# Optimization experiments

Hardware: AMD Instinct MI355X
Metric: run time of the kernel (lower is better)

Reference implementation:

```python
import jax, jax.numpy as jnp
import numpy as np

B, S = 32, 128
NUM_Q, NUM_C = 10000, 256
DIM_K, DIM_E, DIM_CORRECT = 128, 128, 50


def setup_inputs() -> dict:
    key = jax.random.key(0)
    ks = jax.random.split(key, 16)
    w = lambda k, shape: jax.random.normal(k, shape, dtype=jnp.float32) * 0.05
    z = lambda n: jnp.zeros((n,), jnp.float32)
    # q_matrix: sparse binary concept-question map with small smoothing (typical LPKT gamma)
    q_matrix = (jax.random.uniform(ks[4], (NUM_Q + 10, NUM_C)) < 0.03).astype(jnp.float32) + 0.03
    return {
        'e_data': jax.random.randint(ks[0], (B, S), 0, NUM_Q),
        'at_data': jax.random.randint(ks[1], (B, S), 0, 3600),
        'it_data': jax.random.randint(ks[2], (B, S), 0, 43200),
        'a_data': jax.random.uniform(ks[3], (B, S), dtype=jnp.float32),
        'q_matrix': q_matrix,
        'e_E': w(ks[5], (NUM_Q + 10, DIM_K)),
        'at_E': w(ks[6], (3610, DIM_K)),
        'it_E': w(ks[7], (43210, DIM_K)),
        'W1': w(ks[8], (DIM_E + DIM_K + DIM_CORRECT, DIM_K)), 'b1': z(DIM_K),
        'W2': w(ks[9], (4 * DIM_K, DIM_K)), 'b2': z(DIM_K),
        'W3': w(ks[10], (4 * DIM_K, DIM_K)), 'b3': z(DIM_K),
        'W4': w(ks[11], (3 * DIM_K, DIM_K)), 'b4': z(DIM_K),
        'W5': w(ks[12], (DIM_E + DIM_K, DIM_K)), 'b5': z(DIM_K),
        'h0': w(ks[13], (NUM_C, DIM_K)),
    }


def reference(e_data, at_data, it_data, a_data, q_matrix, e_E, at_E, it_E,
              W1, b1, W2, b2, W3, b3, W4, b4, W5, b5, h0):
    Bn, Sn = e_data.shape
    K = W1.shape[1]
    e_emb = e_E[e_data]          # [B,S,K]
    at_emb = at_E[at_data]       # [B,S,K]
    it_emb = it_E[it_data]       # [B,S,K]
    a_rep = jnp.broadcast_to(a_data[:, :, None], (Bn, Sn, DIM_CORRECT))
    all_learning = jnp.concatenate([e_emb, at_emb, a_rep], -1) @ W1 + b1  # [B,S,K]
    q_all = q_matrix[e_data]     # [B,S,C]

    h_init = jnp.broadcast_to(h0, (Bn,) + h0.shape)              # [B,C,K]
    h_tilde_init = jnp.einsum('bc,bck->bk', q_all[:, 0], h_init)  # [B,K]
    learning_init = jnp.zeros((Bn, K), all_learning.dtype)

    xs = jax.tree.map(lambda x: jnp.swapaxes(x, 0, 1),
                      (q_all[:, :-1], q_all[:, 1:], all_learning[:, :-1],
                       it_emb[:, :-1], e_emb[:, 1:]))

    def step(carry, x):
        h, h_tilde, learning_pre = carry
        q_e, q_next, learning, it, e_next = x
        zcat = jnp.concatenate([learning_pre, it, learning, h_tilde], -1)  # [B,4K]
        lg = jnp.tanh(zcat @ W2 + b2)
        gamma_l = jax.nn.sigmoid(zcat @ W3 + b3)
        LG = gamma_l * (lg + 1.0) * 0.5                                    # [B,K]
        LG_tilde = q_e[:, :, None] * LG[:, None, :]                        # [B,C,K] (dropout=eval identity)
        gf_in = jnp.concatenate([h,
                                 jnp.broadcast_to(LG[:, None, :], h.shape),
                                 jnp.broadcast_to(it[:, None, :], h.shape)], -1)
        gamma_f = jax.nn.sigmoid(gf_in @ W4 + b4)                          # [B,C,K]
        h_new = LG_tilde + gamma_f * h
        h_tilde_new = jnp.einsum('bc,bck->bk', q_next, h_new)             # [B,K]
        y = jax.nn.sigmoid(jnp.concatenate([e_next, h_tilde_new], -1) @ W5 + b5).sum(-1) / K
        return (h_new, h_tilde_new, learning), y

    _, ys = jax.lax.scan(step, (h_init, h_tilde_init, learning_init), xs)  # ys: [S-1,B]
    pred = jnp.concatenate([jnp.zeros((Bn, 1), ys.dtype), ys.T], axis=1)    # [B,S]
    return pred
```

## Files before the change

kernel.cpp:

```cpp
#include <hip/hip_runtime.h>
#include <stdint.h>

#define S   128
#define NB  32
#define NC  256
#define DK  128
#define NSL 4
#define HROW 264

typedef __bf16 bf16x8 __attribute__((ext_vector_type(8)));
typedef float  f32x16 __attribute__((ext_vector_type(16)));
typedef unsigned int u32x4 __attribute__((ext_vector_type(4)));
typedef unsigned int u32x2 __attribute__((ext_vector_type(2)));
typedef _Float16 f16x2 __attribute__((ext_vector_type(2)));
static_assert(sizeof(bf16x8) == 16, "bf16x8 size");
static_assert(sizeof(f16x2) == 4, "f16x2 size");

#define OFF_AL   0
#define OFF_HT   OFF_AL
#define OFF_P2   524288
#define OFF_P3   1044480
#define OFF_PS   1564672
#define OFF_PY   2084864
#define OFF_WT5  2654208
#define OFF_CM   2670592

__device__ __forceinline__ float v_exp2(float x){ float r; asm("v_exp_f32 %0, %1" : "=v"(r) : "v"(x)); return r; }
__device__ __forceinline__ float v_rcp (float x){ float r; asm("v_rcp_f32 %0, %1" : "=v"(r) : "v"(x)); return r; }
__device__ __forceinline__ float sigm(float x){ return v_rcp(1.0f + v_exp2(x * -1.4426950408889634f)); }
__device__ __forceinline__ uint32_t pkbf(float lo, float hi){
  uint32_t r; asm("v_cvt_pk_bf16_f32 %0, %1, %2" : "=v"(r) : "v"(lo), "v"(hi)); return r;
}
__device__ __forceinline__ float bfhi(uint32_t w){ return __builtin_bit_cast(float, w & 0xffff0000u); }
__device__ __forceinline__ uint32_t pkh(float a, float b){
  return __builtin_bit_cast(uint32_t, __builtin_amdgcn_cvt_pkrtz(a, b));
}
__device__ __forceinline__ float fdot2u(uint32_t a, uint32_t b, float c){
  return __builtin_amdgcn_fdot2(__builtin_bit_cast(f16x2, a), __builtin_bit_cast(f16x2, b), c, false);
}
__device__ __forceinline__ void barrier_lgkm(){
  asm volatile("s_waitcnt lgkmcnt(0)" ::: "memory");
  __builtin_amdgcn_s_barrier();
}
#define NLOG2E (-1.4426950408889634f)

__global__ __launch_bounds__(512) void k0_al(
    const int* __restrict__ e_data, const int* __restrict__ at_data,
    const float* __restrict__ a_data, const float* __restrict__ e_E,
    const float* __restrict__ at_E, const float* __restrict__ W1,
    const float* __restrict__ b1, float* __restrict__ ws)
{
  __shared__ float ein[32][128];
  __shared__ float atin[32][128];
  int b = blockIdx.x >> 2, q4 = blockIdx.x & 3, t0 = q4 * 32;
  for (int idx = threadIdx.x; idx < 32 * 128; idx += 512) {
    int r = idx >> 7, j = idx & 127;
    int ev  = e_data [b * S + t0 + r];
    int atv = at_data[b * S + t0 + r];
    ein [r][j] = e_E [ev  * DK + j];
    atin[r][j] = at_E[atv * DK + j];
  }
  __syncthreads();
  int j = threadIdx.x & 127, tq = threadIdx.x >> 7;
  float w1s = 0.f;
  for (int d = 0; d < 50; ++d) w1s += W1[(256 + d) * DK + j];
  float acc[8];
#pragma unroll
  for (int u = 0; u < 8; ++u) {
    int t = t0 + tq * 8 + u;
    acc[u] = b1[j] + a_data[b * S + t] * w1s;
  }
  for (int k = 0; k < 128; ++k) {
    float w = W1[k * DK + j];
#pragma unroll
    for (int u = 0; u < 8; ++u) acc[u] += ein[tq * 8 + u][k] * w;
  }
  for (int k = 0; k < 128; ++k) {
    float w = W1[(128 + k) * DK + j];
#pragma unroll
    for (int u = 0; u < 8; ++u) acc[u] += atin[tq * 8 + u][k] * w;
  }
#pragma unroll
  for (int u = 0; u < 8; ++u)
    ws[OFF_AL + (b * S + t0 + tq * 8 + u) * DK + j] = acc[u];
}

__global__ __launch_bounds__(256) void kT_tr(const float* __restrict__ W5, float* __restrict__ ws)
{
  int idx = blockIdx.x * 256 + threadIdx.x;
  int j = idx >> 7, k = idx & 127;
  ws[OFF_WT5 + j * DK + k] = W5[(128 + k) * DK + j];
}

__global__ __launch_bounds__(512) void k1_pre(
    const int* __restrict__ e_data, const int* __restrict__ it_data,
    const float* __restrict__ it_E, const float* __restrict__ e_E,
    const float* __restrict__ W2, const float* __restrict__ b2,
    const float* __restrict__ W3, const float* __restrict__ b3,
    const float* __restrict__ W4, const float* __restrict__ b4,
    const float* __restrict__ W5, const float* __restrict__ b5,
    float* __restrict__ ws)
{
  __shared__ float als[33][128];
  __shared__ float its[32][128];
  __shared__ float ens[32][128];
  int b = blockIdx.x >> 2, sh = blockIdx.x & 3, s0 = sh * 32;
  for (int idx = threadIdx.x; idx < 33 * 128; idx += 512) {
    int r = idx >> 7, j = idx & 127;
    int srow = s0 - 1 + r;
    als[r][j] = (srow >= 0) ? ws[OFF_AL + (b * S + srow) * DK + j] : 0.f;
  }
  for (int idx = threadIdx.x; idx < 32 * 128; idx += 512) {
    int r = idx >> 7, j = idx & 127;
    int itv = it_data[b * S + s0 + r];
    its[r][j] = it_E[itv * DK + j];
    int sg = s0 + r + 1; if (sg > 127) sg = 127;
    int ev = e_data[b * S + sg];
    ens[r][j] = e_E[ev * DK + j];
  }
  __syncthreads();
  int j = threadIdx.x & 127, sq = threadIdx.x >> 7;
  float p2[8], p3[8], pS[8], pY[8];
#pragma unroll
  for (int u = 0; u < 8; ++u) { p2[u] = b2[j]; p3[u] = b3[j]; pS[u] = b4[j]; pY[u] = b5[j]; }
  for (int k = 0; k < 128; ++k) {
    float w2 = W2[k * DK + j], w3 = W3[k * DK + j];
#pragma unroll
    for (int u = 0; u < 8; ++u) { float v = als[sq * 8 + u][k]; p2[u] += v * w2; p3[u] += v * w3; }
  }
  for (int k = 0; k < 128; ++k) {
    float w2 = W2[(128 + k) * DK + j], w3 = W3[(128 + k) * DK + j], w4 = W4[(256 + k) * DK + j];
#pragma unroll
    for (int u = 0; u < 8; ++u) { float v = its[sq * 8 + u][k]; p2[u] += v * w2; p3[u] += v * w3; pS[u] += v * w4; }
  }
  for (int k = 0; k < 128; ++k) {
    float w2 = W2[(256 + k) * DK + j], w3 = W3[(256 + k) * DK + j];
#pragma unroll
    for (int u = 0; u < 8; ++u) { float v = als[sq * 8 + u + 1][k]; p2[u] += v * w2; p3[u] += v * w3; }
  }
  for (int k = 0; k < 128; ++k) {
    float w5 = W5[k * DK + j];
#pragma unroll
    for (int u = 0; u < 8; ++u) pY[u] += ens[sq * 8 + u][k] * w5;
  }
#pragma unroll
  for (int u = 0; u < 8; ++u) {
    int s = s0 + sq * 8 + u;
    if (s < 127) {
      int o = (b * 127 + s) * DK + j;
      ws[OFF_P2 + o] = p2[u]; ws[OFF_P3 + o] = p3[u];
      ws[OFF_PS + o] = pS[u]; ws[OFF_PY + o] = pY[u];
    }
  }
}

__global__ __launch_bounds__(512, 2) void kmain(
    const int* __restrict__ e_data, const float* __restrict__ qmat,
    const float* __restrict__ W2, const float* __restrict__ W3,
    const float* __restrict__ W4, const float* __restrict__ h0,
    float* ws)
{
  __shared__ char     hsb[64 * HROW];
  __shared__ u32x4    W4B[4][8][64];
  __shared__ uint32_t W4Lh[64][128];
  __shared__ float    qbuf[3][64];
  __shared__ float    PST[2][3][128];
  __shared__ uint32_t htldp[64];
  __shared__ uint32_t LGp[64];

  const int bx = blockIdx.x;
  const int b = bx & 31, slice = bx >> 5;
  const int tid = threadIdx.x;
  const int lane = tid & 63, wv = tid >> 6;
  const int ct = wv >> 2, jt = wv & 3;
  const int lo = lane & 31, hi = lane >> 5;
  const int jA = tid >> 2, am = (tid >> 1) & 1, akh = tid & 1;
  const int jloc = jt * 32 + lo;

  uint32_t* cm32 = (uint32_t*)(ws + OFF_CM) + (size_t)b * 2048;

  uint32_t Awh[32];
  {
    const float* Wm = am ? W3 : W2;
#pragma unroll
    for (int i = 0; i < 32; ++i) {
      float w0 = Wm[(384 + akh * 64 + 2 * i) * DK + jA];
      float w1 = Wm[(384 + akh * 64 + 2 * i + 1) * DK + jA];
      Awh[i] = pkh(w0, w1);
    }
  }
  float hm[16];
#pragma unroll
  for (int r = 0; r < 16; ++r) {
    int cl = ct * 32 + (r & 3) + 8 * (r >> 2) + 4 * hi;
    hm[r] = h0[(slice * 64 + cl) * DK + jloc];
  }

  {
    uint32_t* w4b = (uint32_t*)&W4B[0][0][0];
#pragma unroll
    for (int it = 0; it < 16; ++it) {
      int idx = tid + it * 512;
      int w = idx & 3, l = (idx >> 2) & 63, kk = (idx >> 8) & 7, jb = idx >> 11;
      int llo = l & 31, lhi = l >> 5;
      int row = kk * 16 + lhi * 8 + 2 * w, col = jb * 32 + llo;
      w4b[idx] = pkbf(W4[row * DK + col], W4[(row + 1) * DK + col]);
    }
  }
#pragma unroll
  for (int it = 0; it < 16; ++it) {
    int idx = tid + it * 512, kp = idx >> 7, jj = idx & 127;
    W4Lh[kp][jj] = pkh(W4[(128 + 2 * kp) * DK + jj], W4[(128 + 2 * kp + 1) * DK + jj]);
  }
  if (tid < 64) {
    qbuf[0][tid] = qmat[e_data[b * S + 0] * NC + slice * 64 + tid];
    qbuf[1][tid] = qmat[e_data[b * S + 1] * NC + slice * 64 + tid];
  }
  if (tid < 384) {
    int mm = tid >> 7, jj = tid & 127;
    int off = (mm == 0) ? OFF_P2 : (mm == 1) ? OFF_P3 : OFF_PS;
    PST[0][mm][jj] = ws[off + (b * 127 + 0) * DK + jj];
  }
#pragma unroll
  for (int r = 0; r < 16; ++r) {
    int cl = ct * 32 + (r & 3) + 8 * (r >> 2) + 4 * hi;
    *(uint16_t*)(hsb + cl * HROW + jloc * 2) = (uint16_t)pkbf(hm[r], 0.f);
  }
  __syncthreads();

  {
    float ht = 0.f;
#pragma unroll
    for (int r = 0; r < 16; ++r) {
      int cl = ct * 32 + (r & 3) + 8 * (r >> 2) + 4 * hi;
      ht += qbuf[0][cl] * hm[r];
    }
    ht += __shfl_xor(ht, 32);
    if (hi == 0)
      __hip_atomic_store(&cm32[1 * 1024 + (slice * 2 + ct) * 128 + jloc],
                         pkbf(0.f, ht) | 1u, __ATOMIC_RELAXED, __HIP_MEMORY_SCOPE_AGENT);
  }

  float vreg = 0.f;

#pragma unroll 1
  for (int s = 0; s < S - 1; ++s) {
    const int par = s & 1;

    float qld = 0.f, pld = 0.f;
    if (tid >= 448)
      qld = qmat[e_data[b * S + min(s + 2, S - 1)] * NC + slice * 64 + (tid - 448)];
    if (tid >= 128) {
      int mm = (tid - 128) >> 7, jj = tid & 127;
      int off = (mm == 0) ? OFF_P2 : (mm == 1) ? OFF_P3 : OFF_PS;
      pld = ws[off + (b * 127 + min(s + 1, 126)) * DK + jj];
    }

    f32x16 acc;
#pragma unroll
    for (int r = 0; r < 16; ++r) acc[r] = 0.f;
    {
      const char* base = hsb + (ct * 32 + lo) * HROW;
#pragma unroll
      for (int kk = 0; kk < 8; ++kk) {
        u32x2 a0 = *(const u32x2*)(base + kk * 32 + hi * 16);
        u32x2 a1 = *(const u32x2*)(base + kk * 32 + hi * 16 + 8);
        u32x4 af4; af4[0] = a0[0]; af4[1] = a0[1]; af4[2] = a1[0]; af4[3] = a1[1];
        u32x4 bfr = W4B[jt][kk][lane];
        acc = __builtin_amdgcn_mfma_f32_32x32x16_bf16(
            __builtin_bit_cast(bf16x8, af4), __builtin_bit_cast(bf16x8, bfr), acc, 0, 0, 0);
      }
    }

    if (wv < 2) {
      const uint32_t tgt = (uint32_t)(s + 1);
      const uint32_t* src = cm32 + ((s + 1) & 1) * 1024;
      uint32_t g[8];
      for (;;) {
        uint32_t tsum = 0;
#pragma unroll
        for (int p = 0; p < 8; ++p) {
          g[p] = __hip_atomic_load(&src[p * 128 + wv * 64 + lane],
                                   __ATOMIC_RELAXED, __HIP_MEMORY_SCOPE_AGENT);
          tsum += g[p] & 0xffffu;
        }
        if (__all(tsum == 8u * tgt)) break;
        __builtin_amdgcn_s_sleep(1);
      }
      float v = 0.f;
#pragma unroll
      for (int p = 0; p < 8; ++p) v += bfhi(g[p]);
      vreg = v;
      float vn = __shfl_xor(v, 1);
      if (!(lane & 1)) htldp[wv * 32 + (lane >> 1)] = pkh(v, vn);
    }
    barrier_lgkm();

    if (slice == 0 && s > 0 && wv < 2)
      ws[OFF_HT + (b * 127 + (s - 1)) * DK + wv * 64 + lane] = vreg;
    {
      float p0 = 0.f, p1 = 0.f, p2a = 0.f, p3a = 0.f;
#pragma unroll
      for (int t = 0; t < 8; ++t) {
        p0  = fdot2u(htldp[akh * 32 + 4 * t + 0], Awh[4 * t + 0], p0);
        p1  = fdot2u(htldp[akh * 32 + 4 * t + 1], Awh[4 * t + 1], p1);
        p2a = fdot2u(htldp[akh * 32 + 4 * t + 2], Awh[4 * t + 2], p2a);
        p3a = fdot2u(htldp[akh * 32 + 4 * t + 3], Awh[4 * t + 3], p3a);
      }
      float p = (p0 + p1) + (p2a + p3a);
      p += __shfl_xor(p, 1);
      float po = __shfl_xor(p, 2);
      float v2 = am ? po : p;
      float v3 = am ? p : po;
      v2 += PST[par][0][jA];
      v3 += PST[par][1][jA];
      float lg = sigm(v3) * sigm(2.f * v2);
      float lgn = __shfl_xor(lg, 4);
      if ((tid & 7) == 0) LGp[tid >> 3] = pkh(lg, lgn);
    }
    barrier_lgkm();

    if (tid >= 448) qbuf[(s + 2) % 3][tid - 448] = qld;
    if (tid >= 128) {
      int mm = (tid - 128) >> 7, jj = tid & 127;
      PST[(s + 1) & 1][mm][jj] = pld;
    }
    {
      float q0 = 0.f, q1 = 0.f, q2 = 0.f, q3 = 0.f;
#pragma unroll
      for (int t = 0; t < 8; ++t) {
        q0 = fdot2u(LGp[hi * 32 + 4 * t + 0], W4Lh[hi * 32 + 4 * t + 0][jloc], q0);
        q1 = fdot2u(LGp[hi * 32 + 4 * t + 1], W4Lh[hi * 32 + 4 * t + 1][jloc], q1);
        q2 = fdot2u(LGp[hi * 32 + 4 * t + 2], W4Lh[hi * 32 + 4 * t + 2][jloc], q2);
        q3 = fdot2u(LGp[hi * 32 + 4 * t + 3], W4Lh[hi * 32 + 4 * t + 3][jloc], q3);
      }
      float pB = (q0 + q1) + (q2 + q3);
      pB += __shfl_xor(pB, 32);
      float sb = PST[par][2][jloc] + pB;
      float sn = sb * NLOG2E;
      f16x2 l2 = __builtin_bit_cast(f16x2, LGp[jloc >> 1]);
      float lgj = (float)l2[jloc & 1];
      const float* qc = &qbuf[s % 3][0];
      const float* qn = &qbuf[(s + 1) % 3][0];
      float ht = 0.f;
#pragma unroll
      for (int q4 = 0; q4 < 4; ++q4) {
        int cbase = ct * 32 + 8 * q4 + 4 * hi;
        float4 qe4 = *(const float4*)&qc[cbase];
        float4 qn4 = *(const float4*)&qn[cbase];
#pragma unroll
        for (int rr = 0; rr < 4; ++rr) {
          int r = 4 * q4 + rr;
          float qe = (rr == 0) ? qe4.x : (rr == 1) ? qe4.y : (rr == 2) ? qe4.z : qe4.w;
          float qq = (rr == 0) ? qn4.x : (rr == 1) ? qn4.y : (rr == 2) ? qn4.z : qn4.w;
          int cl = cbase + rr;
          float g = v_rcp(1.0f + v_exp2(fmaf(acc[r], NLOG2E, sn)));
          float hn = fmaf(g, hm[r], qe * lgj);
          hm[r] = hn; ht = fmaf(qq, hn, ht);
          *(uint16_t*)(hsb + cl * HROW + jloc * 2) = (uint16_t)pkbf(hn, 0.f);
        }
      }
      ht += __shfl_xor(ht, 32);
      if (hi == 0)
        __hip_atomic_store(&cm32[(s & 1) * 1024 + (slice * 2 + ct) * 128 + jloc],
                           pkbf(0.f, ht) | (uint32_t)(s + 2),
                           __ATOMIC_RELAXED, __HIP_MEMORY_SCOPE_AGENT);
    }
    barrier_lgkm();
  }

  if (slice == 0 && wv < 2) {
    const uint32_t* src = cm32 + 0 * 1024;
    uint32_t g[8];
    for (;;) {
      uint32_t tsum = 0;
#pragma unroll
      for (int p = 0; p < 8; ++p) {
        g[p] = __hip_atomic_load(&src[p * 128 + wv * 64 + lane],
                                 __ATOMIC_RELAXED, __HIP_MEMORY_SCOPE_AGENT);
        tsum += g[p] & 0xffffu;
      }
      if (__all(tsum == 8u * 128u)) break;
      __builtin_amdgcn_s_sleep(1);
    }
    float v = 0.f;
#pragma unroll
    for (int p = 0; p < 8; ++p) v += bfhi(g[p]);
    ws[OFF_HT + (b * 127 + 126) * DK + wv * 64 + lane] = v;
  }
}

__global__ __launch_bounds__(128) void k2_y(const float* __restrict__ ws, float* __restrict__ out)
{
  __shared__ float hts[8][128];
  __shared__ float part[2][8];
  int b = blockIdx.x >> 4, ch = blockIdx.x & 15, s0 = ch * 8;
  int j = threadIdx.x;
#pragma unroll
  for (int u = 0; u < 8; ++u) {
    int s = s0 + u;
    hts[u][j] = (s < 127) ? ws[OFF_HT + (b * 127 + s) * DK + j] : 0.f;
  }
  __syncthreads();
  float acc[8];
#pragma unroll
  for (int u = 0; u < 8; ++u) {
    int s = s0 + u;
    acc[u] = (s < 127) ? ws[OFF_PY + (b * 127 + s) * DK + j] : 0.f;
  }
  const float4* w5 = (const float4*)(ws + OFF_WT5 + j * DK);
#pragma unroll 8
  for (int i = 0; i < 32; ++i) {
    float4 w = w5[i];
#pragma unroll
    for (int u = 0; u < 8; ++u) {
      float4 h4 = *(const float4*)&hts[u][4 * i];
      acc[u] += w.x * h4.x + w.y * h4.y + w.z * h4.z + w.w * h4.w;
    }
  }
#pragma unroll
  for (int u = 0; u < 8; ++u) {
    float v = sigm(acc[u]);
#pragma unroll
    for (int off = 32; off >= 1; off >>= 1) v += __shfl_xor(v, off);
    if ((j & 63) == 0) part[j >> 6][u] = v;
  }
  __syncthreads();
  if (j < 8) {
    int s = s0 + j;
    if (s < 127) out[b * S + s + 1] = (part[0][j] + part[1][j]) * (1.0f / 128.0f);
  }
  if (j == 0 && ch == 0) out[b * S] = 0.f;
}

extern "C" void kernel_launch(void* const* d_in, const int* in_sizes, int n_in,
                              void* d_out, int out_size, void* d_ws, size_t ws_size,
                              hipStream_t stream)
{
  (void)in_sizes; (void)n_in; (void)out_size; (void)ws_size;
  const int*   e_data  = (const int*)  d_in[0];
  const int*   at_data = (const int*)  d_in[1];
  const int*   it_data = (const int*)  d_in[2];
  const float* a_data  = (const float*)d_in[3];
  const float* qmat    = (const float*)d_in[4];
  const float* e_E     = (const float*)d_in[5];
  const float* at_E    = (const float*)d_in[6];
  const float* it_E    = (const float*)d_in[7];
  const float* W1 = (const float*)d_in[8];  const float* b1 = (const float*)d_in[9];
  const float* W2 = (const float*)d_in[10]; const float* b2 = (const float*)d_in[11];
  const float* W3 = (const float*)d_in[12]; const float* b3 = (const float*)d_in[13];
  const float* W4 = (const float*)d_in[14]; const float* b4 = (const float*)d_in[15];
  const float* W5 = (const float*)d_in[16]; const float* b5 = (const float*)d_in[17];
  const float* h0 = (const float*)d_in[18];
  float* ws  = (float*)d_ws;
  float* out = (float*)d_out;

  hipMemsetAsync((char*)d_ws + (size_t)OFF_CM * 4, 0, (size_t)NB * 2 * 8 * 128 * 4, stream);

  k0_al <<<128, 512, 0, stream>>>(e_data, at_data, a_data, e_E, at_E, W1, b1, ws);
  kT_tr <<<64, 256, 0, stream>>>(W5, ws);
  k1_pre<<<128, 512, 0, stream>>>(e_data, it_data, it_E, e_E, W2, b2, W3, b3, W4, b4, W5, b5, ws);
  kmain <<<128, 512, 0, stream>>>(e_data, qmat, W2, W3, W4, h0, ws);
  k2_y  <<<512, 128, 0, stream>>>(ws, out);
}
```

Measured before the change: 414.8 us.

## Process two batch rows per block in recurrent kernel and drop W5 transpose kernel

The main recurrent kernel now handles two batch elements per block, so it launches 64 blocks instead of 128 and shares the W4/W2/W3 weights held in LDS and registers across both rows. It also interleaves two independent MFMA chains and two sets of gate math inside each step. This is meant to hide the latency of the serial per-step chain and of the cross-block spin-waits. Separately, the W5 transpose kernel is removed and k2_y reads W5 directly with strided loads. The cost is twice the per-block work per step and more registers and LDS, which may lengthen each step.

```diff
diff --git a/kernel.cpp b/kernel.cpp
--- a/kernel.cpp
+++ b/kernel.cpp
@@ -22,7 +22,6 @@
 #define OFF_P3   1044480
 #define OFF_PS   1564672
 #define OFF_PY   2084864
-#define OFF_WT5  2654208
 #define OFF_CM   2670592
 
 __device__ __forceinline__ float v_exp2(float x){ float r; asm("v_exp_f32 %0, %1" : "=v"(r) : "v"(x)); return r; }
@@ -83,13 +82,6 @@
 #pragma unroll
   for (int u = 0; u < 8; ++u)
     ws[OFF_AL + (b * S + t0 + tq * 8 + u) * DK + j] = acc[u];
-}
-
-__global__ __launch_bounds__(256) void kT_tr(const float* __restrict__ W5, float* __restrict__ ws)
-{
-  int idx = blockIdx.x * 256 + threadIdx.x;
-  int j = idx >> 7, k = idx & 127;
-  ws[OFF_WT5 + j * DK + k] = W5[(128 + k) * DK + j];
 }
 
 __global__ __launch_bounds__(512) void k1_pre(
@@ -160,24 +152,26 @@
     const float* __restrict__ W4, const float* __restrict__ h0,
     float* ws)
 {
-  __shared__ char     hsb[64 * HROW];
+  __shared__ char     hsb[2][64 * HROW];
   __shared__ u32x4    W4B[4][8][64];
   __shared__ uint32_t W4Lh[64][128];
-  __shared__ float    qbuf[3][64];
-  __shared__ float    PST[2][3][128];
-  __shared__ uint32_t htldp[64];
-  __shared__ uint32_t LGp[64];
+  __shared__ float    qbuf[2][3][64];
+  __shared__ float    PST[2][2][3][128];
+  __shared__ uint32_t htldp[2][64];
+  __shared__ uint32_t LGp[2][64];
 
   const int bx = blockIdx.x;
-  const int b = bx & 31, slice = bx >> 5;
+  const int bp = bx & 15, slice = bx >> 4;
   const int tid = threadIdx.x;
   const int lane = tid & 63, wv = tid >> 6;
   const int ct = wv >> 2, jt = wv & 3;
   const int lo = lane & 31, hi = lane >> 5;
   const int jA = tid >> 2, am = (tid >> 1) & 1, akh = tid & 1;
   const int jloc = jt * 32 + lo;
-
-  uint32_t* cm32 = (uint32_t*)(ws + OFF_CM) + (size_t)b * 2048;
+  const int b0 = bp * 2, b1 = bp * 2 + 1;
+
+  uint32_t* cm0 = (uint32_t*)(ws + OFF_CM) + (size_t)b0 * 2048;
+  uint32_t* cm1 = (uint32_t*)(ws + OFF_CM) + (size_t)b1 * 2048;
 
   uint32_t Awh[32];
   {
@@ -189,11 +183,12 @@
       Awh[i] = pkh(w0, w1);
     }
   }
-  float hm[16];
+  float hm[2][16];
 #pragma unroll
   for (int r = 0; r < 16; ++r) {
     int cl = ct * 32 + (r & 3) + 8 * (r >> 2) + 4 * hi;
-    hm[r] = h0[(slice * 64 + cl) * DK + jloc];
+    float v = h0[(slice * 64 + cl) * DK + jloc];
+    hm[0][r] = v; hm[1][r] = v;
   }
 
   {
@@ -212,32 +207,39 @@
     int idx = tid + it * 512, kp = idx >> 7, jj = idx & 127;
     W4Lh[kp][jj] = pkh(W4[(128 + 2 * kp) * DK + jj], W4[(128 + 2 * kp + 1) * DK + jj]);
   }
-  if (tid < 64) {
-    qbuf[0][tid] = qmat[e_data[b * S + 0] * NC + slice * 64 + tid];
-    qbuf[1][tid] = qmat[e_data[b * S + 1] * NC + slice * 64 + tid];
+  if (tid < 128) {
+    int rr = tid >> 6, t6 = tid & 63;
+    int bb = rr ? b1 : b0;
+    qbuf[rr][0][t6] = qmat[e_data[bb * S + 0] * NC + slice * 64 + t6];
+    qbuf[rr][1][t6] = qmat[e_data[bb * S + 1] * NC + slice * 64 + t6];
   }
   if (tid < 384) {
     int mm = tid >> 7, jj = tid & 127;
     int off = (mm == 0) ? OFF_P2 : (mm == 1) ? OFF_P3 : OFF_PS;
-    PST[0][mm][jj] = ws[off + (b * 127 + 0) * DK + jj];
+    PST[0][0][mm][jj] = ws[off + (b0 * 127 + 0) * DK + jj];
+    PST[1][0][mm][jj] = ws[off + (b1 * 127 + 0) * DK + jj];
   }
 #pragma unroll
   for (int r = 0; r < 16; ++r) {
     int cl = ct * 32 + (r & 3) + 8 * (r >> 2) + 4 * hi;
-    *(uint16_t*)(hsb + cl * HROW + jloc * 2) = (uint16_t)pkbf(hm[r], 0.f);
+    uint16_t v = (uint16_t)pkbf(hm[0][r], 0.f);
+    *(uint16_t*)(&hsb[0][0] + cl * HROW + jloc * 2) = v;
+    *(uint16_t*)(&hsb[1][0] + cl * HROW + jloc * 2) = v;
   }
   __syncthreads();
 
-  {
+#pragma unroll
+  for (int rr = 0; rr < 2; ++rr) {
     float ht = 0.f;
 #pragma unroll
     for (int r = 0; r < 16; ++r) {
       int cl = ct * 32 + (r & 3) + 8 * (r >> 2) + 4 * hi;
-      ht += qbuf[0][cl] * hm[r];
+      ht += qbuf[rr][0][cl] * hm[rr][r];
     }
     ht += __shfl_xor(ht, 32);
+    uint32_t* cm = rr ? cm1 : cm0;
     if (hi == 0)
-      __hip_atomic_store(&cm32[1 * 1024 + (slice * 2 + ct) * 128 + jloc],
+      __hip_atomic_store(&cm[1 * 1024 + (slice * 2 + ct) * 128 + jloc],
                          pkbf(0.f, ht) | 1u, __ATOMIC_RELAXED, __HIP_MEMORY_SCOPE_AGENT);
   }
 
@@ -247,40 +249,56 @@
   for (int s = 0; s < S - 1; ++s) {
     const int par = s & 1;
 
-    float qld = 0.f, pld = 0.f;
-    if (tid >= 448)
-      qld = qmat[e_data[b * S + min(s + 2, S - 1)] * NC + slice * 64 + (tid - 448)];
+    float qld[2] = {0.f, 0.f}, pld[2] = {0.f, 0.f};
+    if (tid >= 448) {
+      int t6 = tid - 448;
+      qld[0] = qmat[e_data[b0 * S + min(s + 2, S - 1)] * NC + slice * 64 + t6];
+      qld[1] = qmat[e_data[b1 * S + min(s + 2, S - 1)] * NC + slice * 64 + t6];
+    }
     if (tid >= 128) {
       int mm = (tid - 128) >> 7, jj = tid & 127;
       int off = (mm == 0) ? OFF_P2 : (mm == 1) ? OFF_P3 : OFF_PS;
-      pld = ws[off + (b * 127 + min(s + 1, 126)) * DK + jj];
-    }
-
-    f32x16 acc;
-#pragma unroll
-    for (int r = 0; r < 16; ++r) acc[r] = 0.f;
+      pld[0] = ws[off + (b0 * 127 + min(s + 1, 126)) * DK + jj];
+      pld[1] = ws[off + (b1 * 127 + min(s + 1, 126)) * DK + jj];
+    }
+
+    f32x16 acc0, acc1;
+#pragma unroll
+    for (int r = 0; r < 16; ++r) { acc0[r] = 0.f; acc1[r] = 0.f; }
     {
-      const char* base = hsb + (ct * 32 + lo) * HROW;
+      const int rowoff = (ct * 32 + lo) * HROW;
 #pragma unroll
       for (int kk = 0; kk < 8; ++kk) {
-        u32x2 a0 = *(const u32x2*)(base + kk * 32 + hi * 16);
-        u32x2 a1 = *(const u32x2*)(base + kk * 32 + hi * 16 + 8);
-        u32x4 af4; af4[0] = a0[0]; af4[1] = a0[1]; af4[2] = a1[0]; af4[3] = a1[1];
         u32x4 bfr = W4B[jt][kk][lane];
-        acc = __builtin_amdgcn_mfma_f32_32x32x16_bf16(
-            __builtin_bit_cast(bf16x8, af4), __builtin_bit_cast(bf16x8, bfr), acc, 0, 0, 0);
-      }
-    }
-
-    if (wv < 2) {
+        {
+          const char* base = &hsb[0][0] + rowoff;
+          u32x2 a0 = *(const u32x2*)(base + kk * 32 + hi * 16);
+          u32x2 a1 = *(const u32x2*)(base + kk * 32 + hi * 16 + 8);
+          u32x4 af4; af4[0] = a0[0]; af4[1] = a0[1]; af4[2] = a1[0]; af4[3] = a1[1];
+          acc0 = __builtin_amdgcn_mfma_f32_32x32x16_bf16(
+              __builtin_bit_cast(bf16x8, af4), __builtin_bit_cast(bf16x8, bfr), acc0, 0, 0, 0);
+        }
+        {
+          const char* base = &hsb[1][0] + rowoff;
+          u32x2 a0 = *(const u32x2*)(base + kk * 32 + hi * 16);
+          u32x2 a1 = *(const u32x2*)(base + kk * 32 + hi * 16 + 8);
+          u32x4 af4; af4[0] = a0[0]; af4[1] = a0[1]; af4[2] = a1[0]; af4[3] = a1[1];
+          acc1 = __builtin_amdgcn_mfma_f32_32x32x16_bf16(
+              __builtin_bit_cast(bf16x8, af4), __builtin_bit_cast(bf16x8, bfr), acc1, 0, 0, 0);
+        }
+      }
+    }
+
+    if (wv < 4) {
+      const int br = wv >> 1, hf = wv & 1;
       const uint32_t tgt = (uint32_t)(s + 1);
-      const uint32_t* src = cm32 + ((s + 1) & 1) * 1024;
+      const uint32_t* src = (br ? cm1 : cm0) + ((s + 1) & 1) * 1024;
       uint32_t g[8];
       for (;;) {
         uint32_t tsum = 0;
 #pragma unroll
         for (int p = 0; p < 8; ++p) {
-          g[p] = __hip_atomic_load(&src[p * 128 + wv * 64 + lane],
+          g[p] = __hip_atomic_load(&src[p * 128 + hf * 64 + lane],
                                    __ATOMIC_RELAXED, __HIP_MEMORY_SCOPE_AGENT);
           tsum += g[p] & 0xffffu;
         }
@@ -292,56 +310,66 @@
       for (int p = 0; p < 8; ++p) v += bfhi(g[p]);
       vreg = v;
       float vn = __shfl_xor(v, 1);
-      if (!(lane & 1)) htldp[wv * 32 + (lane >> 1)] = pkh(v, vn);
+      if (!(lane & 1)) htldp[br][hf * 32 + (lane >> 1)] = pkh(v, vn);
     }
     barrier_lgkm();
 
-    if (slice == 0 && s > 0 && wv < 2)
-      ws[OFF_HT + (b * 127 + (s - 1)) * DK + wv * 64 + lane] = vreg;
-    {
+    if (slice == 0 && s > 0 && wv < 4) {
+      int br = wv >> 1, hf = wv & 1;
+      ws[OFF_HT + ((br ? b1 : b0) * 127 + (s - 1)) * DK + hf * 64 + lane] = vreg;
+    }
+#pragma unroll
+    for (int rr = 0; rr < 2; ++rr) {
       float p0 = 0.f, p1 = 0.f, p2a = 0.f, p3a = 0.f;
 #pragma unroll
       for (int t = 0; t < 8; ++t) {
-        p0  = fdot2u(htldp[akh * 32 + 4 * t + 0], Awh[4 * t + 0], p0);
-        p1  = fdot2u(htldp[akh * 32 + 4 * t + 1], Awh[4 * t + 1], p1);
-        p2a = fdot2u(htldp[akh * 32 + 4 * t + 2], Awh[4 * t + 2], p2a);
-        p3a = fdot2u(htldp[akh * 32 + 4 * t + 3], Awh[4 * t + 3], p3a);
+        p0  = fdot2u(htldp[rr][akh * 32 + 4 * t + 0], Awh[4 * t + 0], p0);
+        p1  = fdot2u(htldp[rr][akh * 32 + 4 * t + 1], Awh[4 * t + 1], p1);
+        p2a = fdot2u(htldp[rr][akh * 32 + 4 * t + 2], Awh[4 * t + 2], p2a);
+        p3a = fdot2u(htldp[rr][akh * 32 + 4 * t + 3], Awh[4 * t + 3], p3a);
       }
       float p = (p0 + p1) + (p2a + p3a);
       p += __shfl_xor(p, 1);
       float po = __shfl_xor(p, 2);
       float v2 = am ? po : p;
       float v3 = am ? p : po;
-      v2 += PST[par][0][jA];
-      v3 += PST[par][1][jA];
+      v2 += PST[rr][par][0][jA];
+      v3 += PST[rr][par][1][jA];
       float lg = sigm(v3) * sigm(2.f * v2);
       float lgn = __shfl_xor(lg, 4);
-      if ((tid & 7) == 0) LGp[tid >> 3] = pkh(lg, lgn);
+      if ((tid & 7) == 0) LGp[rr][tid >> 3] = pkh(lg, lgn);
     }
     barrier_lgkm();
 
-    if (tid >= 448) qbuf[(s + 2) % 3][tid - 448] = qld;
+    if (tid >= 448) {
+      qbuf[0][(s + 2) % 3][tid - 448] = qld[0];
+      qbuf[1][(s + 2) % 3][tid - 448] = qld[1];
+    }
     if (tid >= 128) {
       int mm = (tid - 128) >> 7, jj = tid & 127;
-      PST[(s + 1) & 1][mm][jj] = pld;
-    }
-    {
+      PST[0][(s + 1) & 1][mm][jj] = pld[0];
+      PST[1][(s + 1) & 1][mm][jj] = pld[1];
+    }
+#pragma unroll
+    for (int rr = 0; rr < 2; ++rr) {
       float q0 = 0.f, q1 = 0.f, q2 = 0.f, q3 = 0.f;
 #pragma unroll
       for (int t = 0; t < 8; ++t) {
-        q0 = fdot2u(LGp[hi * 32 + 4 * t + 0], W4Lh[hi * 32 + 4 * t + 0][jloc], q0);
-        q1 = fdot2u(LGp[hi * 32 + 4 * t + 1], W4Lh[hi * 32 + 4 * t + 1][jloc], q1);
-        q2 = fdot2u(LGp[hi * 32 + 4 * t + 2], W4Lh[hi * 32 + 4 * t + 2][jloc], q2);
-        q3 = fdot2u(LGp[hi * 32 + 4 * t + 3], W4Lh[hi * 32 + 4 * t + 3][jloc], q3);
+        q0 = fdot2u(LGp[rr][hi * 32 + 4 * t + 0], W4Lh[hi * 32 + 4 * t + 0][jloc], q0);
+        q1 = fdot2u(LGp[rr][hi * 32 + 4 * t + 1], W4Lh[hi * 32 + 4 * t + 1][jloc], q1);
+        q2 = fdot2u(LGp[rr][hi * 32 + 4 * t + 2], W4Lh[hi * 32 + 4 * t + 2][jloc], q2);
+        q3 = fdot2u(LGp[rr][hi * 32 + 4 * t + 3], W4Lh[hi * 32 + 4 * t + 3][jloc], q3);
       }
       float pB = (q0 + q1) + (q2 + q3);
       pB += __shfl_xor(pB, 32);
-      float sb = PST[par][2][jloc] + pB;
+      float sb = PST[rr][par][2][jloc] + pB;
       float sn = sb * NLOG2E;
-      f16x2 l2 = __builtin_bit_cast(f16x2, LGp[jloc >> 1]);
+      f16x2 l2 = __builtin_bit_cast(f16x2, LGp[rr][jloc >> 1]);
       float lgj = (float)l2[jloc & 1];
-      const float* qc = &qbuf[s % 3][0];
-      const float* qn = &qbuf[(s + 1) % 3][0];
+      const float* qc = &qbuf[rr][s % 3][0];
+      const float* qn = &qbuf[rr][(s + 1) % 3][0];
+      f32x16 accr = rr ? acc1 : acc0;
+      char* hb = &hsb[rr][0];
       float ht = 0.f;
 #pragma unroll
       for (int q4 = 0; q4 < 4; ++q4) {
@@ -349,34 +377,36 @@
         float4 qe4 = *(const float4*)&qc[cbase];
         float4 qn4 = *(const float4*)&qn[cbase];
 #pragma unroll
-        for (int rr = 0; rr < 4; ++rr) {
-          int r = 4 * q4 + rr;
-          float qe = (rr == 0) ? qe4.x : (rr == 1) ? qe4.y : (rr == 2) ? qe4.z : qe4.w;
-          float qq = (rr == 0) ? qn4.x : (rr == 1) ? qn4.y : (rr == 2) ? qn4.z : qn4.w;
-          int cl = cbase + rr;
-          float g = v_rcp(1.0f + v_exp2(fmaf(acc[r], NLOG2E, sn)));
-          float hn = fmaf(g, hm[r], qe * lgj);
-          hm[r] = hn; ht = fmaf(qq, hn, ht);
-          *(uint16_t*)(hsb + cl * HROW + jloc * 2) = (uint16_t)pkbf(hn, 0.f);
+        for (int rx = 0; rx < 4; ++rx) {
+          int r = 4 * q4 + rx;
+          float qe = (rx == 0) ? qe4.x : (rx == 1) ? qe4.y : (rx == 2) ? qe4.z : qe4.w;
+          float qq = (rx == 0) ? qn4.x : (rx == 1) ? qn4.y : (rx == 2) ? qn4.z : qn4.w;
+          int cl = cbase + rx;
+          float g = v_rcp(1.0f + v_exp2(fmaf(accr[r], NLOG2E, sn)));
+          float hn = fmaf(g, hm[rr][r], qe * lgj);
+          hm[rr][r] = hn; ht = fmaf(qq, hn, ht);
+          *(uint16_t*)(hb + cl * HROW + jloc * 2) = (uint16_t)pkbf(hn, 0.f);
         }
       }
       ht += __shfl_xor(ht, 32);
+      uint32_t* cm = rr ? cm1 : cm0;
       if (hi == 0)
-        __hip_atomic_store(&cm32[(s & 1) * 1024 + (slice * 2 + ct) * 128 + jloc],
+        __hip_atomic_store(&cm[(s & 1) * 1024 + (slice * 2 + ct) * 128 + jloc],
                            pkbf(0.f, ht) | (uint32_t)(s + 2),
                            __ATOMIC_RELAXED, __HIP_MEMORY_SCOPE_AGENT);
     }
     barrier_lgkm();
   }
 
-  if (slice == 0 && wv < 2) {
-    const uint32_t* src = cm32 + 0 * 1024;
+  if (slice == 0 && wv < 4) {
+    const int br = wv >> 1, hf = wv & 1;
+    const uint32_t* src = (br ? cm1 : cm0) + 0 * 1024;
     uint32_t g[8];
     for (;;) {
       uint32_t tsum = 0;
 #pragma unroll
       for (int p = 0; p < 8; ++p) {
-        g[p] = __hip_atomic_load(&src[p * 128 + wv * 64 + lane],
+        g[p] = __hip_atomic_load(&src[p * 128 + hf * 64 + lane],
                                  __ATOMIC_RELAXED, __HIP_MEMORY_SCOPE_AGENT);
         tsum += g[p] & 0xffffu;
       }
@@ -386,11 +416,13 @@
     float v = 0.f;
 #pragma unroll
     for (int p = 0; p < 8; ++p) v += bfhi(g[p]);
-    ws[OFF_HT + (b * 127 + 126) * DK + wv * 64 + lane] = v;
-  }
-}
-
-__global__ __launch_bounds__(128) void k2_y(const float* __restrict__ ws, float* __restrict__ out)
+    ws[OFF_HT + ((br ? b1 : b0) * 127 + 126) * DK + hf * 64 + lane] = v;
+  }
+}
+
+__global__ __launch_bounds__(128) void k2_y(const float* __restrict__ ws,
+                                            const float* __restrict__ W5,
+                                            float* __restrict__ out)
 {
   __shared__ float hts[8][128];
   __shared__ float part[2][8];
@@ -408,15 +440,11 @@
     int s = s0 + u;
     acc[u] = (s < 127) ? ws[OFF_PY + (b * 127 + s) * DK + j] : 0.f;
   }
-  const float4* w5 = (const float4*)(ws + OFF_WT5 + j * DK);
-#pragma unroll 8
-  for (int i = 0; i < 32; ++i) {
-    float4 w = w5[i];
-#pragma unroll
-    for (int u = 0; u < 8; ++u) {
-      float4 h4 = *(const float4*)&hts[u][4 * i];
-      acc[u] += w.x * h4.x + w.y * h4.y + w.z * h4.z + w.w * h4.w;
-    }
+#pragma unroll 4
+  for (int k = 0; k < 128; ++k) {
+    float w = W5[(128 + k) * DK + j];
+#pragma unroll
+    for (int u = 0; u < 8; ++u) acc[u] += w * hts[u][k];
   }
 #pragma unroll
   for (int u = 0; u < 8; ++u) {
@@ -458,8 +486,7 @@
   hipMemsetAsync((char*)d_ws + (size_t)OFF_CM * 4, 0, (size_t)NB * 2 * 8 * 128 * 4, stream);
 
   k0_al <<<128, 512, 0, stream>>>(e_data, at_data, a_data, e_E, at_E, W1, b1, ws);
-  kT_tr <<<64, 256, 0, stream>>>(W5, ws);
   k1_pre<<<128, 512, 0, stream>>>(e_data, it_data, it_E, e_E, W2, b2, W3, b3, W4, b4, W5, b5, ws);
-  kmain <<<128, 512, 0, stream>>>(e_data, qmat, W2, W3, W4, h0, ws);
-  k2_y  <<<512, 128, 0, stream>>>(ws, out);
-}
+  kmain <<<64, 512, 0, stream>>>(e_data, qmat, W2, W3, W4, h0, ws);
+  k2_y  <<<512, 128, 0, stream>>>(ws, W5, out);
+}
```

Result: slower. 628.3 us (+51.4%).
